# Kernel tuning notes

Hardware: AMD Instinct MI355X
Metric: run time of the kernel (lower is better)

## Reference

```python
import jax, jax.numpy as jnp
import numpy as np

N_EMB = 250_000   # param.num_embeddings
D     = 128       # param.embedding_dim
N_IDX = 65_536    # number of traced ids this step (with duplicates)
LR    = 1e-3
B1, B2 = 0.9, 0.999
EPS   = 1e-8


def setup_inputs() -> dict:
    key = jax.random.key(0)
    k1, k2, k3, k4, k5, k6 = jax.random.split(key, 6)
    idx = jax.random.randint(k1, (N_IDX,), 0, N_EMB)                      # gathered ids, duplicates likely
    grad = 0.01 * jax.random.normal(k2, (N_IDX, D), dtype=jnp.float32)   # per-occurrence grads
    emb = jax.random.normal(k3, (N_EMB, D), dtype=jnp.float32)           # embedding table (emb.tensor)
    state_step = jnp.zeros((N_EMB,), dtype=jnp.float32)                  # Adam step counts
    state_mem = 0.01 * jax.random.normal(k4, (N_EMB, D), dtype=jnp.float32)   # first moment
    state_power = 0.01 * jax.random.uniform(k5, (N_EMB, D), dtype=jnp.float32)  # second moment (>=0)
    return {"idx": idx, "grad": grad, "emb": emb, "state_step": state_step,
            "state_mem": state_mem, "state_power": state_power}


def reference(idx, grad, emb, state_step, state_mem, state_power):
    # --- unique_grads: dedup ids, mean of duplicate grads (unique + index_add_ / counts) ---
    # Done via scatter-add into table space (same math at touched rows, identity elsewhere;
    # avoids dynamic-shape jnp.unique under jit).
    counts = jnp.zeros((N_EMB,), dtype=grad.dtype).at[idx].add(1.0)          # [N]
    gsum = jnp.zeros((N_EMB, D), dtype=grad.dtype).at[idx].add(grad)         # [N, D]
    mask = counts > 0                                                        # touched rows
    gmean = gsum / jnp.maximum(counts, 1.0)[:, None]                         # grad_values

    # --- fused sparse Adam on touched rows ---
    step_new = state_step + mask.astype(state_step.dtype)                    # state_step + 1
    mem_new = jnp.where(mask[:, None], B1 * state_mem + (1.0 - B1) * gmean, state_mem)
    power_new = jnp.where(mask[:, None], B2 * state_power + (1.0 - B2) * gmean * gmean, state_power)

    # bias correction (safe denominators on untouched rows)
    denom1 = jnp.where(mask, 1.0 - jnp.power(B1, step_new), 1.0)
    denom2 = jnp.where(mask, 1.0 - jnp.power(B2, step_new), 1.0)
    mem_corr = mem_new / denom1[:, None]
    power_corr = jnp.where(mask[:, None], power_new / denom2[:, None], 1.0)  # double-where: keep sqrt grad finite
    std = LR * mem_corr / (jnp.sqrt(power_corr) + EPS)

    # --- scatter writeback into embedding table ---
    emb_new = jnp.where(mask[:, None], emb - std, emb)
    return emb_new
```

## Files before the change

kernel.cpp:

```cpp
#include <hip/hip_runtime.h>

#define ADAM_B1 0.9f
#define ADAM_B2 0.999f
#define ADAM_LR 1e-3f
#define ADAM_EPS 1e-8f

__global__ void k_count_zero(const int* __restrict__ idx, float* __restrict__ out,
                             unsigned* __restrict__ counts, int n_idx, int D) {
    int wave = (int)((blockIdx.x * (unsigned)blockDim.x + threadIdx.x) >> 6);
    int lane = threadIdx.x & 63;
    if (wave >= n_idx) return;
    int row = idx[wave];
    if (lane == 0) atomicAdd(&counts[row], 1u);
    float2* o = (float2*)(out + (long long)row * D);
    int nv = D >> 1;
    for (int c = lane; c < nv; c += 64)
        o[c] = make_float2(0.f, 0.f);
}

__global__ void k_scatter(const int* __restrict__ idx, const float* __restrict__ grad,
                          float* __restrict__ out, long long total, int D) {
    long long i = (long long)blockIdx.x * blockDim.x + threadIdx.x;
    if (i >= total) return;
    int occ = (int)(i / D);
    int col = (int)(i - (long long)occ * D);
    int row = idx[occ];
    atomicAdd(&out[(long long)row * D + col], grad[i]);
}

__global__ void k_adam(const float* __restrict__ emb,
                       const float* __restrict__ step_,
                       const float* __restrict__ mem_,
                       const float* __restrict__ pow_,
                       const unsigned* __restrict__ counts,
                       float* __restrict__ out, int n_emb, int D) {
    int wave = (int)((blockIdx.x * (unsigned)blockDim.x + threadIdx.x) >> 6);
    int lane = threadIdx.x & 63;
    if (wave >= n_emb) return;
    long long base = (long long)wave * D;
    unsigned cnt = counts[wave];
    const float2* e2 = (const float2*)(emb + base);
    float2* o2 = (float2*)(out + base);
    int nv = D >> 1;
    if (cnt == 0) {
        for (int c = lane; c < nv; c += 64) o2[c] = e2[c];
        return;
    }
    float inv_cnt = 1.0f / (float)cnt;
    float stepn = step_[wave] + 1.0f;
    float d1 = 1.0f - powf(ADAM_B1, stepn);
    float d2 = 1.0f - powf(ADAM_B2, stepn);
    float inv_d1 = 1.0f / d1;
    float inv_d2 = 1.0f / d2;
    const float2* m2 = (const float2*)(mem_ + base);
    const float2* p2 = (const float2*)(pow_ + base);
    for (int c = lane; c < nv; c += 64) {
        float2 g = o2[c];
        g.x *= inv_cnt; g.y *= inv_cnt;
        float2 m = m2[c];
        float2 p = p2[c];
        float2 e = e2[c];
        float mx = ADAM_B1 * m.x + (1.0f - ADAM_B1) * g.x;
        float my = ADAM_B1 * m.y + (1.0f - ADAM_B1) * g.y;
        float px = ADAM_B2 * p.x + (1.0f - ADAM_B2) * g.x * g.x;
        float py = ADAM_B2 * p.y + (1.0f - ADAM_B2) * g.y * g.y;
        float sx = ADAM_LR * (mx * inv_d1) / (sqrtf(px * inv_d2) + ADAM_EPS);
        float sy = ADAM_LR * (my * inv_d1) / (sqrtf(py * inv_d2) + ADAM_EPS);
        o2[c] = make_float2(e.x - sx, e.y - sy);
    }
}

extern "C" void kernel_launch(void* const* d_in, const int* in_sizes, int n_in,
                              void* d_out, int out_size, void* d_ws, size_t ws_size,
                              hipStream_t stream) {
    const int*   idx   = (const int*)d_in[0];
    const float* grad  = (const float*)d_in[1];
    const float* emb   = (const float*)d_in[2];
    const float* step_ = (const float*)d_in[3];
    const float* mem_  = (const float*)d_in[4];
    const float* pow_  = (const float*)d_in[5];
    float* out = (float*)d_out;

    int n_idx = in_sizes[0];
    int n_emb = in_sizes[3];
    int D     = in_sizes[1] / n_idx;

    unsigned* counts = (unsigned*)d_ws;
    hipMemsetAsync(counts, 0, (size_t)n_emb * sizeof(unsigned), stream);

    const int blk = 256;

    long long t1 = (long long)n_idx * 64;
    k_count_zero<<<(int)((t1 + blk - 1) / blk), blk, 0, stream>>>(idx, out, counts, n_idx, D);

    long long total = (long long)n_idx * D;
    k_scatter<<<(int)((total + blk - 1) / blk), blk, 0, stream>>>(idx, grad, out, total, D);

    long long t3 = (long long)n_emb * 64;
    k_adam<<<(int)((t3 + blk - 1) / blk), blk, 0, stream>>>(emb, step_, mem_, pow_, counts, out, n_emb, D);
}
```

Before: 412.1 us.

## Replace atomic scatter with per-row linked lists and fuse gather into Adam

Builds per-row linked lists of occurrence indices with atomicExch. The Adam kernel then walks each touched row's list to sum and average the gradients directly, which removes the float atomicAdd scatter pass and the zeroing pass over the output rows. It also widens accesses to float4 with 32 lanes per row and replaces powf with exp2f using precomputed log2 constants. The risk is that the summation order of duplicate gradients now depends on list order, and the list walk does serial dependent loads per row.

Measured after the change: 373.1 us. 1.1x faster.

```diff
diff --git a/kernel.cpp b/kernel.cpp
--- a/kernel.cpp
+++ b/kernel.cpp
@@ -5,68 +5,84 @@
 #define ADAM_LR 1e-3f
 #define ADAM_EPS 1e-8f
 
-__global__ void k_count_zero(const int* __restrict__ idx, float* __restrict__ out,
-                             unsigned* __restrict__ counts, int n_idx, int D) {
-    int wave = (int)((blockIdx.x * (unsigned)blockDim.x + threadIdx.x) >> 6);
-    int lane = threadIdx.x & 63;
-    if (wave >= n_idx) return;
-    int row = idx[wave];
-    if (lane == 0) atomicAdd(&counts[row], 1u);
-    float2* o = (float2*)(out + (long long)row * D);
-    int nv = D >> 1;
-    for (int c = lane; c < nv; c += 64)
-        o[c] = make_float2(0.f, 0.f);
+__global__ void k_build_list(const int* __restrict__ idx, int* __restrict__ head,
+                             int* __restrict__ next_, int n_idx) {
+    int i = blockIdx.x * blockDim.x + threadIdx.x;
+    if (i >= n_idx) return;
+    int row = idx[i];
+    next_[i] = atomicExch(&head[row], i);
 }
 
-__global__ void k_scatter(const int* __restrict__ idx, const float* __restrict__ grad,
-                          float* __restrict__ out, long long total, int D) {
-    long long i = (long long)blockIdx.x * blockDim.x + threadIdx.x;
-    if (i >= total) return;
-    int occ = (int)(i / D);
-    int col = (int)(i - (long long)occ * D);
-    int row = idx[occ];
-    atomicAdd(&out[(long long)row * D + col], grad[i]);
-}
+__global__ void k_adam_fused(const float* __restrict__ emb,
+                             const float* __restrict__ step_,
+                             const float* __restrict__ mem_,
+                             const float* __restrict__ pow_,
+                             const float* __restrict__ grad,
+                             const int* __restrict__ head,
+                             const int* __restrict__ next_,
+                             float* __restrict__ out, int n_emb, int D) {
+    int gid = blockIdx.x * blockDim.x + threadIdx.x;
+    int row = gid >> 5;
+    int lane = threadIdx.x & 31;
+    if (row >= n_emb) return;
+    long long base = (long long)row * D;
+    const float4* e4 = (const float4*)(emb + base);
+    float4* o4 = (float4*)(out + base);
+    int nv = D >> 2;
 
-__global__ void k_adam(const float* __restrict__ emb,
-                       const float* __restrict__ step_,
-                       const float* __restrict__ mem_,
-                       const float* __restrict__ pow_,
-                       const unsigned* __restrict__ counts,
-                       float* __restrict__ out, int n_emb, int D) {
-    int wave = (int)((blockIdx.x * (unsigned)blockDim.x + threadIdx.x) >> 6);
-    int lane = threadIdx.x & 63;
-    if (wave >= n_emb) return;
-    long long base = (long long)wave * D;
-    unsigned cnt = counts[wave];
-    const float2* e2 = (const float2*)(emb + base);
-    float2* o2 = (float2*)(out + base);
-    int nv = D >> 1;
-    if (cnt == 0) {
-        for (int c = lane; c < nv; c += 64) o2[c] = e2[c];
+    int h = head[row];
+    if (h < 0) {
+        for (int c = lane; c < nv; c += 32) o4[c] = e4[c];
         return;
     }
-    float inv_cnt = 1.0f / (float)cnt;
-    float stepn = step_[wave] + 1.0f;
-    float d1 = 1.0f - powf(ADAM_B1, stepn);
-    float d2 = 1.0f - powf(ADAM_B2, stepn);
-    float inv_d1 = 1.0f / d1;
-    float inv_d2 = 1.0f / d2;
-    const float2* m2 = (const float2*)(mem_ + base);
-    const float2* p2 = (const float2*)(pow_ + base);
-    for (int c = lane; c < nv; c += 64) {
-        float2 g = o2[c];
-        g.x *= inv_cnt; g.y *= inv_cnt;
-        float2 m = m2[c];
-        float2 p = p2[c];
-        float2 e = e2[c];
-        float mx = ADAM_B1 * m.x + (1.0f - ADAM_B1) * g.x;
-        float my = ADAM_B1 * m.y + (1.0f - ADAM_B1) * g.y;
-        float px = ADAM_B2 * p.x + (1.0f - ADAM_B2) * g.x * g.x;
-        float py = ADAM_B2 * p.y + (1.0f - ADAM_B2) * g.y * g.y;
-        float sx = ADAM_LR * (mx * inv_d1) / (sqrtf(px * inv_d2) + ADAM_EPS);
-        float sy = ADAM_LR * (my * inv_d1) / (sqrtf(py * inv_d2) + ADAM_EPS);
-        o2[c] = make_float2(e.x - sx, e.y - sy);
+
+    float cnt = 0.0f;
+    for (int c = lane; c < nv; c += 32) {
+        float4 g = make_float4(0.f, 0.f, 0.f, 0.f);
+        int p = h;
+        float k = 0.0f;
+        while (p >= 0) {
+            const float4* g4 = (const float4*)(grad + (long long)p * D);
+            float4 gv = g4[c];
+            g.x += gv.x; g.y += gv.y; g.z += gv.z; g.w += gv.w;
+            k += 1.0f;
+            p = next_[p];
+        }
+        cnt = k;
+
+        float inv_cnt = 1.0f / cnt;
+        g.x *= inv_cnt; g.y *= inv_cnt; g.z *= inv_cnt; g.w *= inv_cnt;
+
+        float stepn = step_[row] + 1.0f;
+        const float L2B1 = -0.15200309344504997f;
+        const float L2B2 = -0.0014434592066161948f;
+        float d1 = 1.0f - exp2f(stepn * L2B1);
+        float d2 = 1.0f - exp2f(stepn * L2B2);
+        float inv_d1 = 1.0f / d1;
+        float inv_d2 = 1.0f / d2;
+
+        const float4* m4 = (const float4*)(mem_ + base);
+        const float4* p4 = (const float4*)(pow_ + base);
+        float4 m = m4[c];
+        float4 pv = p4[c];
+        float4 e = e4[c];
+
+        float4 r;
+        {
+            float mx = ADAM_B1 * m.x + (1.0f - ADAM_B1) * g.x;
+            float px = ADAM_B2 * pv.x + (1.0f - ADAM_B2) * g.x * g.x;
+            r.x = e.x - ADAM_LR * (mx * inv_d1) / (sqrtf(px * inv_d2) + ADAM_EPS);
+            float my = ADAM_B1 * m.y + (1.0f - ADAM_B1) * g.y;
+            float py = ADAM_B2 * pv.y + (1.0f - ADAM_B2) * g.y * g.y;
+            r.y = e.y - ADAM_LR * (my * inv_d1) / (sqrtf(py * inv_d2) + ADAM_EPS);
+            float mz = ADAM_B1 * m.z + (1.0f - ADAM_B1) * g.z;
+            float pz = ADAM_B2 * pv.z + (1.0f - ADAM_B2) * g.z * g.z;
+            r.z = e.z - ADAM_LR * (mz * inv_d1) / (sqrtf(pz * inv_d2) + ADAM_EPS);
+            float mw = ADAM_B1 * m.w + (1.0f - ADAM_B1) * g.w;
+            float pw = ADAM_B2 * pv.w + (1.0f - ADAM_B2) * g.w * g.w;
+            r.w = e.w - ADAM_LR * (mw * inv_d1) / (sqrtf(pw * inv_d2) + ADAM_EPS);
+        }
+        o4[c] = r;
     }
 }
 
@@ -85,17 +101,15 @@
     int n_emb = in_sizes[3];
     int D     = in_sizes[1] / n_idx;
 
-    unsigned* counts = (unsigned*)d_ws;
-    hipMemsetAsync(counts, 0, (size_t)n_emb * sizeof(unsigned), stream);
+    int* head  = (int*)d_ws;
+    int* next_ = head + n_emb;
+
+    hipMemsetAsync(head, 0xFF, (size_t)n_emb * sizeof(int), stream);
 
     const int blk = 256;
+    k_build_list<<<(n_idx + blk - 1) / blk, blk, 0, stream>>>(idx, head, next_, n_idx);
 
-    long long t1 = (long long)n_idx * 64;
-    k_count_zero<<<(int)((t1 + blk - 1) / blk), blk, 0, stream>>>(idx, out, counts, n_idx, D);
-
-    long long total = (long long)n_idx * D;
-    k_scatter<<<(int)((total + blk - 1) / blk), blk, 0, stream>>>(idx, grad, out, total, D);
-
-    long long t3 = (long long)n_emb * 64;
-    k_adam<<<(int)((t3 + blk - 1) / blk), blk, 0, stream>>>(emb, step_, mem_, pow_, counts, out, n_emb, D);
+    long long threads = (long long)n_emb * 32;
+    k_adam_fused<<<(int)((threads + blk - 1) / blk), blk, 0, stream>>>(
+        emb, step_, mem_, pow_, grad, head, next_, out, n_emb, D);
 }
```
